# Kernel optimization log

Hardware: AMD Instinct MI355X
Metric: run time of the kernel (lower is better)

Reference implementation:

```python
import jax, jax.numpy as jnp
import numpy as np

KNOTS = 16
BN_EPS = 1e-5  # flax BatchNorm default


def _normalize_spline_params(W, H, D):
    # widths/heights sum to 1 over the [0,1] hypercube; slopes positive
    dx = jax.nn.softmax(W, axis=-1)          # (N, d, K) bin widths
    dy = jax.nn.softmax(H, axis=-1)          # (N, d, K) bin heights
    sl = jax.nn.softplus(D)                  # (N, d, K-1) interior knot slopes
    return dx, dy, sl


def _gather_bin(a, idx):
    # a: (N, d, K'), idx: (N, d) -> (N, d)
    return jnp.take_along_axis(a, idx[..., None], axis=-1)[..., 0]


def _rqs_forward(t, dx, dy, sl):
    """Rational-quadratic spline on [0,1] (Durkan et al. 2019); identity outside.
    t: (N, d); dx, dy: (N, d, K); sl: (N, d, K-1).
    Returns y: (N, d), log_det: (N,)."""
    K = dx.shape[-1]
    zero = jnp.zeros_like(dx[..., :1])
    one = jnp.ones_like(dx[..., :1])
    xk = jnp.concatenate([zero, jnp.cumsum(dx, axis=-1)], axis=-1)   # (N, d, K+1) knot x
    yk = jnp.concatenate([zero, jnp.cumsum(dy, axis=-1)], axis=-1)   # (N, d, K+1) knot y
    dk = jnp.concatenate([one, sl, one], axis=-1)                    # (N, d, K+1) knot slopes

    in_bounds = (t >= 0.0) & (t <= 1.0)
    tc = jnp.clip(t, 0.0, 1.0)
    # per-element bin search (vectorized searchsorted)
    idx = jnp.clip(jnp.sum((tc[..., None] >= xk).astype(jnp.int32), axis=-1) - 1, 0, K - 1)

    xk_b = _gather_bin(xk, idx)
    yk_b = _gather_bin(yk, idx)
    dx_b = _gather_bin(dx, idx)
    dy_b = _gather_bin(dy, idx)
    d0 = _gather_bin(dk, idx)
    d1 = _gather_bin(dk, idx + 1)

    xi = (tc - xk_b) / dx_b            # position within bin, in [0,1]
    s = dy_b / dx_b                    # bin mean slope
    xi1m = xi * (1.0 - xi)
    den = s + (d0 + d1 - 2.0 * s) * xi1m
    y_in = yk_b + dy_b * (s * xi * xi + d0 * xi1m) / den
    dydx = s * s * (d1 * xi * xi + 2.0 * s * xi1m + d0 * (1.0 - xi) ** 2) / (den * den)

    y = jnp.where(in_bounds, y_in, t)
    log_det = jnp.sum(jnp.where(in_bounds, jnp.log(dydx), 0.0), axis=1)  # (N,)
    return y, log_det


def setup_inputs() -> dict:
    key = jax.random.key(0)
    ks = jax.random.split(key, 8)
    N, D, C = 65536, 64, 16
    d = D // 2
    spline_dim = 3 * KNOTS - 1
    cin = d + C           # conditioner input width: hstack(xc, c)
    H1, H2 = 128, 128     # layers=(128,128)

    def dense(k, fi, fo):
        return (jax.random.normal(k, (fi, fo), jnp.float32) / np.float32(np.sqrt(fi)))

    return {
        "x": jax.random.uniform(ks[0], (N, D), jnp.float32),
        "c": jax.random.normal(ks[1], (N, C), jnp.float32),
        "bn_scale": jnp.ones((cin,), jnp.float32),
        "bn_bias": jnp.zeros((cin,), jnp.float32),
        "bn_mean": 0.1 * jax.random.normal(ks[2], (cin,), jnp.float32),
        "bn_var": jax.random.uniform(ks[3], (cin,), jnp.float32, minval=0.5, maxval=1.5),
        "W0": dense(ks[4], cin, H1), "b0": jnp.zeros((H1,), jnp.float32),
        "W1": dense(ks[5], H1, H2), "b1": jnp.zeros((H2,), jnp.float32),
        "W2": dense(ks[6], H2, d * spline_dim), "b2": jnp.zeros((d * spline_dim,), jnp.float32),
    }


def reference(x, c, bn_scale, bn_bias, bn_mean, bn_var, W0, b0, W1, b1, W2, b2):
    N, D = x.shape
    d = D // 2
    xt, xc = x[:, :d], x[:, d:]
    h = jnp.hstack((xc, c))
    # BatchNorm in eval mode (use_running_average=True)
    h = (h - bn_mean) * jax.lax.rsqrt(bn_var + BN_EPS) * bn_scale + bn_bias
    h = jax.nn.swish(h @ W0 + b0)
    h = jax.nn.swish(h @ W1 + b1)
    p = (h @ W2 + b2).reshape(N, d, 3 * KNOTS - 1)
    dx, dy, sl = _normalize_spline_params(
        p[..., :KNOTS], p[..., KNOTS:2 * KNOTS], p[..., 2 * KNOTS:])
    yt, log_det = _rqs_forward(xt, dx, dy, sl)
    y = jnp.hstack((yt, xc))
    return y, log_det
```

## Files before the change

### kernel.cpp

```cpp
#include <hip/hip_runtime.h>
#include <math.h>

#define BN_EPS 1e-5f
#define ROWS 64

typedef __attribute__((ext_vector_type(8))) short short8;
typedef __attribute__((ext_vector_type(4))) float float4v;

__device__ __forceinline__ unsigned short f2bf(float f) {
    union { float f; unsigned int u; } v; v.f = f;
    unsigned int r = v.u + 0x7FFF + ((v.u >> 16) & 1);
    return (unsigned short)(r >> 16);
}
__device__ __forceinline__ float softplus_f(float v) {
    float r = log1pf(__expf(-fabsf(v)));
    return v > 0.f ? v + r : r;
}
__device__ __forceinline__ float swish_f(float a) {
    return a / (1.f + __expf(-a));
}

__global__ void prep_weights(const float* __restrict__ W0, const float* __restrict__ W1,
                             const float* __restrict__ W2, const float* __restrict__ b2,
                             unsigned short* __restrict__ Wt0, unsigned short* __restrict__ Wt1,
                             unsigned short* __restrict__ Wt2, float* __restrict__ b2p) {
    int e = blockIdx.x * 256 + threadIdx.x;
    if (e < 128 * 64) {
        int n = e >> 6, k = e & 63;
        Wt0[e] = f2bf(k < 48 ? W0[k * 128 + n] : 0.f);
        return;
    }
    e -= 128 * 64;
    if (e < 128 * 128) {
        int n = e >> 7, k = e & 127;
        Wt1[e] = f2bf(W1[k * 128 + n]);
        return;
    }
    e -= 128 * 128;
    if (e < 1536 * 128) {
        int col = e >> 7, k = e & 127;
        int d = col / 48, j = col - d * 48;
        Wt2[e] = f2bf(j < 47 ? W2[k * 1504 + d * 47 + j] : 0.f);
        return;
    }
    e -= 1536 * 128;
    if (e < 32 * 48) {
        int d = e / 48, j = e - d * 48;
        b2p[e] = (j < 47) ? b2[d * 47 + j] : 0.f;
    }
}

__launch_bounds__(256, 4)
__global__ void nsc_mfma(const float* __restrict__ x, const float* __restrict__ c,
                         const float* __restrict__ bn_scale, const float* __restrict__ bn_bias,
                         const float* __restrict__ bn_mean, const float* __restrict__ bn_var,
                         const unsigned short* __restrict__ Wt0, const float* __restrict__ b0,
                         const unsigned short* __restrict__ Wt1, const float* __restrict__ b1,
                         const unsigned short* __restrict__ Wt2, const float* __restrict__ b2p,
                         float* __restrict__ out, int N) {
    __shared__ __align__(16) char smem[38912];
    unsigned short* h0 = (unsigned short*)smem;
    unsigned short* h2 = (unsigned short*)smem;
    unsigned short* h1 = (unsigned short*)(smem + 17408);
    float*          ldp = (float*)(smem + 17408 + 20480);

    const int tid  = threadIdx.x;
    const int lane = tid & 63;
    const int l    = lane & 15;
    const int q    = lane >> 4;
    const int wu   = __builtin_amdgcn_readfirstlane(tid >> 6);
    const int r0   = blockIdx.x * ROWS;
    float* pw = (float*)(smem + 17408) + wu * (64 * 20);

    for (int idx = tid; idx < 64 * 64; idx += 256) {
        int r = idx >> 6, j = idx & 63;
        float h = 0.f;
        if (j < 48) {
            int row = r0 + r;
            float v = (j < 32) ? x[(size_t)row * 64 + 32 + j] : c[(size_t)row * 16 + (j - 32)];
            h = (v - bn_mean[j]) * rsqrtf(bn_var[j] + BN_EPS) * bn_scale[j] + bn_bias[j];
        }
        h0[r * 72 + j] = f2bf(h);
    }
    for (int idx = tid; idx < 64 * 32; idx += 256) {
        int r = idx >> 5, j = idx & 31;
        out[(size_t)(r0 + r) * 64 + 32 + j] = x[(size_t)(r0 + r) * 64 + 32 + j];
    }
    __syncthreads();

    {
        float4v acc[2][4];
        float4v z = {0.f, 0.f, 0.f, 0.f};
        #pragma unroll
        for (int nt = 0; nt < 2; ++nt)
            #pragma unroll
            for (int mt = 0; mt < 4; ++mt) acc[nt][mt] = z;
        #pragma unroll
        for (int ks = 0; ks < 2; ++ks) {
            short8 a[4];
            #pragma unroll
            for (int mt = 0; mt < 4; ++mt)
                a[mt] = *(const short8*)(h0 + (mt * 16 + l) * 72 + ks * 32 + (q << 3));
            #pragma unroll
            for (int nt = 0; nt < 2; ++nt) {
                int n0 = (wu * 2 + nt) * 16;
                short8 b = *(const short8*)(Wt0 + (n0 + l) * 64 + ks * 32 + (q << 3));
                #pragma unroll
                for (int mt = 0; mt < 4; ++mt)
                    acc[nt][mt] = __builtin_amdgcn_mfma_f32_16x16x32_bf16(a[mt], b, acc[nt][mt], 0, 0, 0);
            }
        }
        #pragma unroll
        for (int nt = 0; nt < 2; ++nt) {
            int n0 = (wu * 2 + nt) * 16;
            float bb = b0[n0 + l];
            #pragma unroll
            for (int mt = 0; mt < 4; ++mt)
                #pragma unroll
                for (int r = 0; r < 4; ++r)
                    h1[(mt * 16 + q * 4 + r) * 136 + n0 + l] = f2bf(swish_f(acc[nt][mt][r] + bb));
        }
    }
    __syncthreads();

    {
        float4v acc[2][4];
        float4v z = {0.f, 0.f, 0.f, 0.f};
        #pragma unroll
        for (int nt = 0; nt < 2; ++nt)
            #pragma unroll
            for (int mt = 0; mt < 4; ++mt) acc[nt][mt] = z;
        #pragma unroll
        for (int ks = 0; ks < 4; ++ks) {
            short8 a[4];
            #pragma unroll
            for (int mt = 0; mt < 4; ++mt)
                a[mt] = *(const short8*)(h1 + (mt * 16 + l) * 136 + ks * 32 + (q << 3));
            #pragma unroll
            for (int nt = 0; nt < 2; ++nt) {
                int n0 = (wu * 2 + nt) * 16;
                short8 b = *(const short8*)(Wt1 + (n0 + l) * 128 + ks * 32 + (q << 3));
                #pragma unroll
                for (int mt = 0; mt < 4; ++mt)
                    acc[nt][mt] = __builtin_amdgcn_mfma_f32_16x16x32_bf16(a[mt], b, acc[nt][mt], 0, 0, 0);
            }
        }
        #pragma unroll
        for (int nt = 0; nt < 2; ++nt) {
            int n0 = (wu * 2 + nt) * 16;
            float bb = b1[n0 + l];
            #pragma unroll
            for (int mt = 0; mt < 4; ++mt)
                #pragma unroll
                for (int r = 0; r < 4; ++r)
                    h2[(mt * 16 + q * 4 + r) * 136 + n0 + l] = f2bf(swish_f(acc[nt][mt][r] + bb));
        }
    }
    __syncthreads();

    float ld_local = 0.f;
    float yreg[8];
    for (int pass = 0; pass < 8; ++pass) {
        const int d = wu * 8 + pass;
        float4v acc[3][4];
        float4v z = {0.f, 0.f, 0.f, 0.f};
        #pragma unroll
        for (int jt = 0; jt < 3; ++jt)
            #pragma unroll
            for (int smt = 0; smt < 4; ++smt) acc[jt][smt] = z;
        #pragma unroll
        for (int ks = 0; ks < 4; ++ks) {
            short8 bf[4];
            #pragma unroll
            for (int smt = 0; smt < 4; ++smt)
                bf[smt] = *(const short8*)(h2 + (smt * 16 + l) * 136 + ks * 32 + (q << 3));
            #pragma unroll
            for (int jt = 0; jt < 3; ++jt) {
                short8 a = *(const short8*)(Wt2 + (size_t)(d * 48 + jt * 16 + l) * 128 + ks * 32 + (q << 3));
                #pragma unroll
                for (int smt = 0; smt < 4; ++smt)
                    acc[jt][smt] = __builtin_amdgcn_mfma_f32_16x16x32_bf16(a, bf[smt], acc[jt][smt], 0, 0, 0);
            }
        }

        float t  = x[(size_t)(r0 + lane) * 64 + d];
        bool inb = (t >= 0.f) && (t <= 1.f);
        float tc = fminf(fmaxf(t, 0.f), 1.f);
        float pr[16];

        {
            float4v bj = *(const float4v*)(b2p + d * 48 + (q << 2));
            #pragma unroll
            for (int smt = 0; smt < 4; ++smt)
                *(float4v*)(pw + (smt * 16 + l) * 20 + (q << 2)) = acc[0][smt] + bj;
            asm volatile("s_waitcnt lgkmcnt(0)" ::: "memory");
            #pragma unroll
            for (int c2 = 0; c2 < 4; ++c2)
                *(float4v*)(pr + c2 * 4) = *(const float4v*)(pw + lane * 20 + c2 * 4);
        }
        float mW = pr[0];
        #pragma unroll
        for (int i = 1; i < 16; ++i) mW = fmaxf(mW, pr[i]);
        float sW = 0.f;
        #pragma unroll
        for (int i = 0; i < 16; ++i) { pr[i] = __expf(pr[i] - mW); sW += pr[i]; }
        float invW = 1.f / sW;
        float cum = 0.f, xkb = 0.f, dxb = pr[0] * invW;
        int idx = 0;
        #pragma unroll
        for (int i = 0; i < 16; ++i) {
            float dxi = pr[i] * invW;
            bool cnd = (tc >= cum);
            idx = cnd ? i   : idx;
            xkb = cnd ? cum : xkb;
            dxb = cnd ? dxi : dxb;
            cum += dxi;
        }

        {
            float4v bj = *(const float4v*)(b2p + d * 48 + 16 + (q << 2));
            #pragma unroll
            for (int smt = 0; smt < 4; ++smt)
                *(float4v*)(pw + (smt * 16 + l) * 20 + (q << 2)) = acc[1][smt] + bj;
            asm volatile("s_waitcnt lgkmcnt(0)" ::: "memory");
            #pragma unroll
            for (int c2 = 0; c2 < 4; ++c2)
                *(float4v*)(pr + c2 * 4) = *(const float4v*)(pw + lane * 20 + c2 * 4);
        }
        float mH = pr[0];
        #pragma unroll
        for (int i = 1; i < 16; ++i) mH = fmaxf(mH, pr[i]);
        float sH = 0.f;
        #pragma unroll
        for (int i = 0; i < 16; ++i) { pr[i] = __expf(pr[i] - mH); sH += pr[i]; }
        float invH = 1.f / sH;
        float ykb = 0.f, dyb = pr[0] * invH;
        #pragma unroll
        for (int i = 0; i < 16; ++i) {
            float dyi = pr[i] * invH;
            ykb += (i < idx) ? dyi : 0.f;
            dyb  = (i == idx) ? dyi : dyb;
        }

        {
            float4v bj = *(const float4v*)(b2p + d * 48 + 32 + (q << 2));
            #pragma unroll
            for (int smt = 0; smt < 4; ++smt)
                *(float4v*)(pw + (smt * 16 + l) * 20 + (q << 2)) = acc[2][smt] + bj;
            asm volatile("s_waitcnt lgkmcnt(0)" ::: "memory");
            #pragma unroll
            for (int c2 = 0; c2 < 4; ++c2)
                *(float4v*)(pr + c2 * 4) = *(const float4v*)(pw + lane * 20 + c2 * 4);
        }
        float a0 = 0.f, a1 = 0.f;
        #pragma unroll
        for (int i = 0; i < 15; ++i) {
            a0 = (i == idx - 1) ? pr[i] : a0;
            a1 = (i == idx)     ? pr[i] : a1;
        }
        float d0 = (idx == 0)  ? 1.f : softplus_f(a0);
        float d1 = (idx == 15) ? 1.f : softplus_f(a1);

        float xi  = (tc - xkb) / dxb;
        float s   = dyb / dxb;
        float xim = 1.f - xi;
        float x1m = xi * xim;
        float den = s + (d0 + d1 - 2.f * s) * x1m;
        float y_in = ykb + dyb * (s * xi * xi + d0 * x1m) / den;
        float dydx = s * s * (d1 * xi * xi + 2.f * s * x1m + d0 * xim * xim) / (den * den);

        yreg[pass] = inb ? y_in : t;
        ld_local += inb ? __logf(dydx) : 0.f;
    }

    {
        float4v* o = (float4v*)(out + (size_t)(r0 + lane) * 64 + wu * 8);
        o[0] = *(const float4v*)(yreg);
        o[1] = *(const float4v*)(yreg + 4);
    }
    ldp[wu * 64 + lane] = ld_local;
    __syncthreads();
    if (tid < 64) {
        out[(size_t)N * 64 + r0 + tid] =
            ldp[tid] + ldp[64 + tid] + ldp[128 + tid] + ldp[192 + tid];
    }
}

extern "C" void kernel_launch(void* const* d_in, const int* in_sizes, int n_in,
                              void* d_out, int out_size, void* d_ws, size_t ws_size,
                              hipStream_t stream) {
    const float* x        = (const float*)d_in[0];
    const float* c        = (const float*)d_in[1];
    const float* bn_scale = (const float*)d_in[2];
    const float* bn_bias  = (const float*)d_in[3];
    const float* bn_mean  = (const float*)d_in[4];
    const float* bn_var   = (const float*)d_in[5];
    const float* W0       = (const float*)d_in[6];
    const float* b0       = (const float*)d_in[7];
    const float* W1       = (const float*)d_in[8];
    const float* b1       = (const float*)d_in[9];
    const float* W2       = (const float*)d_in[10];
    const float* b2       = (const float*)d_in[11];
    float* out = (float*)d_out;

    unsigned short* Wt0 = (unsigned short*)d_ws;
    unsigned short* Wt1 = Wt0 + 128 * 64;
    unsigned short* Wt2 = Wt1 + 128 * 128;
    float*          b2p = (float*)(Wt2 + 1536 * 128);

    const int N = in_sizes[0] / 64;
    const int prep_elems = 128 * 64 + 128 * 128 + 1536 * 128 + 32 * 48;
    prep_weights<<<(prep_elems + 255) / 256, 256, 0, stream>>>(
        W0, W1, W2, b2, Wt0, Wt1, Wt2, b2p);
    nsc_mfma<<<N / ROWS, 256, 0, stream>>>(x, c, bn_scale, bn_bias, bn_mean, bn_var,
                                           Wt0, b0, Wt1, b1, Wt2, b2p, out, N);
}
```

Measured before the change: 172.0 us.

## Fold BatchNorm into W0, LDS-transpose prep, hoist h2 fragments, vectorize copies

```diff
diff --git a/kernel.cpp b/kernel.cpp
--- a/kernel.cpp
+++ b/kernel.cpp
@@ -21,40 +21,82 @@
 }
 
 __global__ void prep_weights(const float* __restrict__ W0, const float* __restrict__ W1,
-                             const float* __restrict__ W2, const float* __restrict__ b2,
+                             const float* __restrict__ W2, const float* __restrict__ b0,
+                             const float* __restrict__ b2,
+                             const float* __restrict__ bn_scale, const float* __restrict__ bn_bias,
+                             const float* __restrict__ bn_mean, const float* __restrict__ bn_var,
                              unsigned short* __restrict__ Wt0, unsigned short* __restrict__ Wt1,
-                             unsigned short* __restrict__ Wt2, float* __restrict__ b2p) {
-    int e = blockIdx.x * 256 + threadIdx.x;
-    if (e < 128 * 64) {
-        int n = e >> 6, k = e & 63;
-        Wt0[e] = f2bf(k < 48 ? W0[k * 128 + n] : 0.f);
+                             unsigned short* __restrict__ Wt2, float* __restrict__ b0p,
+                             float* __restrict__ b2p) {
+    __shared__ float lds[64 * 129 + 128];
+    const int bid = blockIdx.x, tid = threadIdx.x;
+    if (bid < 26) {
+        const float* src;
+        int rstride, c0;
+        bool remap;
+        if (bid < 24) { src = W2; rstride = 1504; c0 = bid * 64; remap = true; }
+        else          { src = W1; rstride = 128;  c0 = (bid - 24) * 64; remap = false; }
+        const int cl = tid & 63;
+        const int cd = c0 + cl;
+        int scol = cd;
+        bool valid = true;
+        if (remap) {
+            int dd = cd / 48, j = cd - dd * 48;
+            valid = (j < 47);
+            scol = dd * 47 + j;
+        }
+        #pragma unroll 4
+        for (int it = 0; it < 32; ++it) {
+            int k = (tid >> 6) + it * 4;
+            lds[cl * 129 + k] = valid ? src[k * rstride + scol] : 0.f;
+        }
+        __syncthreads();
+        unsigned short* dst = (bid < 24) ? Wt2 : Wt1;
+        #pragma unroll 4
+        for (int it = 0; it < 32; ++it) {
+            int cl2 = (tid >> 7) + it * 2;
+            int k = tid & 127;
+            dst[(size_t)(c0 + cl2) * 128 + k] = f2bf(lds[cl2 * 129 + k]);
+        }
         return;
     }
-    e -= 128 * 64;
-    if (e < 128 * 128) {
-        int n = e >> 7, k = e & 127;
-        Wt1[e] = f2bf(W1[k * 128 + n]);
+    if (bid == 26) {
+        float* a   = lds + 48 * 129;
+        float* bsh = a + 48;
+        if (tid < 48) {
+            float av = bn_scale[tid] * rsqrtf(bn_var[tid] + BN_EPS);
+            a[tid] = av;
+            bsh[tid] = bn_bias[tid] - bn_mean[tid] * av;
+        }
+        for (int idx = tid; idx < 48 * 128; idx += 256) {
+            int k = idx >> 7, n = idx & 127;
+            lds[k * 129 + n] = W0[k * 128 + n];
+        }
+        __syncthreads();
+        #pragma unroll 4
+        for (int it = 0; it < 32; ++it) {
+            int n = (tid >> 6) + it * 4;
+            int k = tid & 63;
+            float v = (k < 48) ? lds[k * 129 + n] * a[k] : 0.f;
+            Wt0[n * 64 + k] = f2bf(v);
+        }
+        if (tid < 128) {
+            float s = b0[tid];
+            #pragma unroll
+            for (int k = 0; k < 48; ++k) s += bsh[k] * lds[k * 129 + tid];
+            b0p[tid] = s;
+        }
         return;
     }
-    e -= 128 * 128;
-    if (e < 1536 * 128) {
-        int col = e >> 7, k = e & 127;
-        int d = col / 48, j = col - d * 48;
-        Wt2[e] = f2bf(j < 47 ? W2[k * 1504 + d * 47 + j] : 0.f);
-        return;
-    }
-    e -= 1536 * 128;
-    if (e < 32 * 48) {
-        int d = e / 48, j = e - d * 48;
-        b2p[e] = (j < 47) ? b2[d * 47 + j] : 0.f;
+    for (int e = tid; e < 32 * 48; e += 256) {
+        int dd = e / 48, j = e - dd * 48;
+        b2p[e] = (j < 47) ? b2[dd * 47 + j] : 0.f;
     }
 }
 
 __launch_bounds__(256, 4)
 __global__ void nsc_mfma(const float* __restrict__ x, const float* __restrict__ c,
-                         const float* __restrict__ bn_scale, const float* __restrict__ bn_bias,
-                         const float* __restrict__ bn_mean, const float* __restrict__ bn_var,
-                         const unsigned short* __restrict__ Wt0, const float* __restrict__ b0,
+                         const unsigned short* __restrict__ Wt0, const float* __restrict__ b0p,
                          const unsigned short* __restrict__ Wt1, const float* __restrict__ b1,
                          const unsigned short* __restrict__ Wt2, const float* __restrict__ b2p,
                          float* __restrict__ out, int N) {
@@ -77,14 +119,14 @@
         float h = 0.f;
         if (j < 48) {
             int row = r0 + r;
-            float v = (j < 32) ? x[(size_t)row * 64 + 32 + j] : c[(size_t)row * 16 + (j - 32)];
-            h = (v - bn_mean[j]) * rsqrtf(bn_var[j] + BN_EPS) * bn_scale[j] + bn_bias[j];
+            h = (j < 32) ? x[(size_t)row * 64 + 32 + j] : c[(size_t)row * 16 + (j - 32)];
         }
         h0[r * 72 + j] = f2bf(h);
     }
-    for (int idx = tid; idx < 64 * 32; idx += 256) {
-        int r = idx >> 5, j = idx & 31;
-        out[(size_t)(r0 + r) * 64 + 32 + j] = x[(size_t)(r0 + r) * 64 + 32 + j];
+    for (int idx = tid; idx < 64 * 8; idx += 256) {
+        int r = idx >> 3, ch = idx & 7;
+        float4v v = *(const float4v*)(x + (size_t)(r0 + r) * 64 + 32 + ch * 4);
+        *(float4v*)(out + (size_t)(r0 + r) * 64 + 32 + ch * 4) = v;
     }
     __syncthreads();
 
@@ -113,7 +155,7 @@
         #pragma unroll
         for (int nt = 0; nt < 2; ++nt) {
             int n0 = (wu * 2 + nt) * 16;
-            float bb = b0[n0 + l];
+            float bb = b0p[n0 + l];
             #pragma unroll
             for (int mt = 0; mt < 4; ++mt)
                 #pragma unroll
@@ -157,42 +199,37 @@
         }
     }
     __syncthreads();
+
+    short8 bf[4][4];
+    #pragma unroll
+    for (int ks = 0; ks < 4; ++ks)
+        #pragma unroll
+        for (int smt = 0; smt < 4; ++smt)
+            bf[ks][smt] = *(const short8*)(h2 + (smt * 16 + l) * 136 + ks * 32 + (q << 3));
 
     float ld_local = 0.f;
     float yreg[8];
     for (int pass = 0; pass < 8; ++pass) {
         const int d = wu * 8 + pass;
-        float4v acc[3][4];
-        float4v z = {0.f, 0.f, 0.f, 0.f};
-        #pragma unroll
-        for (int jt = 0; jt < 3; ++jt)
-            #pragma unroll
-            for (int smt = 0; smt < 4; ++smt) acc[jt][smt] = z;
-        #pragma unroll
-        for (int ks = 0; ks < 4; ++ks) {
-            short8 bf[4];
-            #pragma unroll
-            for (int smt = 0; smt < 4; ++smt)
-                bf[smt] = *(const short8*)(h2 + (smt * 16 + l) * 136 + ks * 32 + (q << 3));
-            #pragma unroll
-            for (int jt = 0; jt < 3; ++jt) {
-                short8 a = *(const short8*)(Wt2 + (size_t)(d * 48 + jt * 16 + l) * 128 + ks * 32 + (q << 3));
-                #pragma unroll
-                for (int smt = 0; smt < 4; ++smt)
-                    acc[jt][smt] = __builtin_amdgcn_mfma_f32_16x16x32_bf16(a, bf[smt], acc[jt][smt], 0, 0, 0);
-            }
-        }
-
-        float t  = x[(size_t)(r0 + lane) * 64 + d];
+        float t = x[(size_t)(r0 + lane) * 64 + d];
         bool inb = (t >= 0.f) && (t <= 1.f);
         float tc = fminf(fmaxf(t, 0.f), 1.f);
         float pr[16];
+        float4v z = {0.f, 0.f, 0.f, 0.f};
 
         {
+            float4v acc[4] = {z, z, z, z};
+            #pragma unroll
+            for (int ks = 0; ks < 4; ++ks) {
+                short8 a = *(const short8*)(Wt2 + (size_t)(d * 48 + l) * 128 + ks * 32 + (q << 3));
+                #pragma unroll
+                for (int smt = 0; smt < 4; ++smt)
+                    acc[smt] = __builtin_amdgcn_mfma_f32_16x16x32_bf16(a, bf[ks][smt], acc[smt], 0, 0, 0);
+            }
             float4v bj = *(const float4v*)(b2p + d * 48 + (q << 2));
             #pragma unroll
             for (int smt = 0; smt < 4; ++smt)
-                *(float4v*)(pw + (smt * 16 + l) * 20 + (q << 2)) = acc[0][smt] + bj;
+                *(float4v*)(pw + (smt * 16 + l) * 20 + (q << 2)) = acc[smt] + bj;
             asm volatile("s_waitcnt lgkmcnt(0)" ::: "memory");
             #pragma unroll
             for (int c2 = 0; c2 < 4; ++c2)
@@ -218,10 +255,18 @@
         }
 
         {
+            float4v acc[4] = {z, z, z, z};
+            #pragma unroll
+            for (int ks = 0; ks < 4; ++ks) {
+                short8 a = *(const short8*)(Wt2 + (size_t)(d * 48 + 16 + l) * 128 + ks * 32 + (q << 3));
+                #pragma unroll
+                for (int smt = 0; smt < 4; ++smt)
+                    acc[smt] = __builtin_amdgcn_mfma_f32_16x16x32_bf16(a, bf[ks][smt], acc[smt], 0, 0, 0);
+            }
             float4v bj = *(const float4v*)(b2p + d * 48 + 16 + (q << 2));
             #pragma unroll
             for (int smt = 0; smt < 4; ++smt)
-                *(float4v*)(pw + (smt * 16 + l) * 20 + (q << 2)) = acc[1][smt] + bj;
+                *(float4v*)(pw + (smt * 16 + l) * 20 + (q << 2)) = acc[smt] + bj;
             asm volatile("s_waitcnt lgkmcnt(0)" ::: "memory");
             #pragma unroll
             for (int c2 = 0; c2 < 4; ++c2)
@@ -243,23 +288,26 @@
         }
 
         {
+            float4v acc[4] = {z, z, z, z};
+            #pragma unroll
+            for (int ks = 0; ks < 4; ++ks) {
+                short8 a = *(const short8*)(Wt2 + (size_t)(d * 48 + 32 + l) * 128 + ks * 32 + (q << 3));
+                #pragma unroll
+                for (int smt = 0; smt < 4; ++smt)
+                    acc[smt] = __builtin_amdgcn_mfma_f32_16x16x32_bf16(a, bf[ks][smt], acc[smt], 0, 0, 0);
+            }
             float4v bj = *(const float4v*)(b2p + d * 48 + 32 + (q << 2));
             #pragma unroll
             for (int smt = 0; smt < 4; ++smt)
-                *(float4v*)(pw + (smt * 16 + l) * 20 + (q << 2)) = acc[2][smt] + bj;
+                *(float4v*)(pw + (smt * 16 + l) * 20 + (q << 2)) = acc[smt] + bj;
             asm volatile("s_waitcnt lgkmcnt(0)" ::: "memory");
-            #pragma unroll
-            for (int c2 = 0; c2 < 4; ++c2)
-                *(float4v*)(pr + c2 * 4) = *(const float4v*)(pw + lane * 20 + c2 * 4);
-        }
-        float a0 = 0.f, a1 = 0.f;
-        #pragma unroll
-        for (int i = 0; i < 15; ++i) {
-            a0 = (i == idx - 1) ? pr[i] : a0;
-            a1 = (i == idx)     ? pr[i] : a1;
-        }
-        float d0 = (idx == 0)  ? 1.f : softplus_f(a0);
-        float d1 = (idx == 15) ? 1.f : softplus_f(a1);
+        }
+        int i0 = (idx > 0)  ? idx - 1 : 0;
+        int i1 = (idx < 15) ? idx     : 14;
+        float pa0 = pw[lane * 20 + i0];
+        float pa1 = pw[lane * 20 + i1];
+        float d0 = (idx == 0)  ? 1.f : softplus_f(pa0);
+        float d1 = (idx == 15) ? 1.f : softplus_f(pa1);
 
         float xi  = (tc - xkb) / dxb;
         float s   = dyb / dxb;
@@ -307,11 +355,11 @@
     unsigned short* Wt1 = Wt0 + 128 * 64;
     unsigned short* Wt2 = Wt1 + 128 * 128;
     float*          b2p = (float*)(Wt2 + 1536 * 128);
+    float*          b0p = b2p + 32 * 48;
 
     const int N = in_sizes[0] / 64;
-    const int prep_elems = 128 * 64 + 128 * 128 + 1536 * 128 + 32 * 48;
-    prep_weights<<<(prep_elems + 255) / 256, 256, 0, stream>>>(
-        W0, W1, W2, b2, Wt0, Wt1, Wt2, b2p);
-    nsc_mfma<<<N / ROWS, 256, 0, stream>>>(x, c, bn_scale, bn_bias, bn_mean, bn_var,
-                                           Wt0, b0, Wt1, b1, Wt2, b2p, out, N);
-}
+    prep_weights<<<28, 256, 0, stream>>>(W0, W1, W2, b0, b2,
+                                         bn_scale, bn_bias, bn_mean, bn_var,
+                                         Wt0, Wt1, Wt2, b0p, b2p);
+    nsc_mfma<<<N / ROWS, 256, 0, stream>>>(x, c, Wt0, b0p, Wt1, b1, Wt2, b2p, out, N);
+}
```

Result: slower. 248.9 us (+44.7%).
